# Optimization experiments

Hardware: AMD Instinct MI355X
Metric: run time of the kernel (lower is better)

## Reference

```python
import jax, jax.numpy as jnp
import numpy as np

IN_FEATURES = 4096
OUT_FEATURES = 8192
LUT_SIZE = 65536  # 256 * 256 two-level codebook


def setup_inputs() -> dict:
    key = jax.random.key(0)
    k_x, k_b, k_f, k_s, k_l = jax.random.split(key, 5)
    x = jax.random.normal(k_x, (2, 256, IN_FEATURES), dtype=jnp.float32)
    base_idx = jax.random.randint(k_b, (OUT_FEATURES, IN_FEATURES), 0, 256, dtype=jnp.int32)
    fine_idx = jax.random.randint(k_f, (OUT_FEATURES, IN_FEATURES), 0, 256, dtype=jnp.int32)
    scale = jax.random.uniform(k_s, (OUT_FEATURES, 1), dtype=jnp.float32)
    lut = jax.random.normal(k_l, (LUT_SIZE,), dtype=jnp.float32)
    return {"x": x, "base_idx": base_idx, "fine_idx": fine_idx, "scale": scale, "lut": lut}


def reference(x, base_idx, fine_idx, scale, lut):
    # Two-level LUT dequant: combined 16-bit index = base*256 + fine
    combined_idx = base_idx * 256 + fine_idx              # [out, in] int32
    weights = lut[combined_idx] * scale                   # [out, in] fp32, per-row scale
    # F.linear(x, weights) == x @ weights.T
    return jnp.einsum('bsi,oi->bso', x, weights)
```

## Files before the change

### kernel.cpp

```cpp
#include <hip/hip_runtime.h>

typedef unsigned short ushort_t;
typedef unsigned int   uint32;
typedef __attribute__((ext_vector_type(8)))  short short8;
typedef __attribute__((ext_vector_type(4)))  float floatx4;
typedef __attribute__((ext_vector_type(16))) float floatx16;

#define IN_F   4096
#define OUT_F  8192
#define M_TOT  512

__device__ __forceinline__ ushort_t f2bf(float f) {
    uint32 u = __builtin_bit_cast(uint32, f);
    u += 0x7FFFu + ((u >> 16) & 1u);
    return (ushort_t)(u >> 16);
}
__device__ __forceinline__ uint32 pack2bf(float a, float b) {
    return (uint32)f2bf(a) | ((uint32)f2bf(b) << 16);
}

__global__ void cvt_x_kernel(const float* __restrict__ x, ushort_t* __restrict__ xb) {
    const int g  = blockIdx.x * 256 + threadIdx.x;
    const int r  = g >> 9;
    const int k0 = (g & 511) * 8;
    float4 v0 = *(const float4*)(x + (size_t)r * IN_F + k0);
    float4 v1 = *(const float4*)(x + (size_t)r * IN_F + k0 + 4);
    short8 s;
    s[0] = (short)f2bf(v0.x); s[1] = (short)f2bf(v0.y);
    s[2] = (short)f2bf(v0.z); s[3] = (short)f2bf(v0.w);
    s[4] = (short)f2bf(v1.x); s[5] = (short)f2bf(v1.y);
    s[6] = (short)f2bf(v1.z); s[7] = (short)f2bf(v1.w);
    const int mt = r >> 5;
    const int kt = k0 >> 4;
    ushort_t* dst = xb + ((size_t)(mt * 256 + kt) * 32 + (r & 31)) * 16 + (k0 & 15);
    *(short8*)dst = s;
}

__global__ __launch_bounds__(1024, 4)
void fused_kernel(const ushort_t* __restrict__ xb, const int* __restrict__ base_idx,
                  const int* __restrict__ fine_idx, const float* __restrict__ lut,
                  const float* __restrict__ scale, float* __restrict__ out)
{
    __shared__ ushort_t sh_lut[65536];
    __shared__ ushort_t sh_w[2][32 * 128];

    const int tid  = threadIdx.x;
    const int nblk = blockIdx.x;

    for (int i = tid * 4; i < 65536; i += 4096) {
        float4 v = *(const float4*)(lut + i);
        *(uint32*)&sh_lut[i]     = pack2bf(v.x, v.y);
        *(uint32*)&sh_lut[i + 2] = pack2bf(v.z, v.w);
    }

    const int colr = tid >> 5;
    const int kq   = (tid & 31) * 4;
    const int4* bp = (const int4*)(base_idx + (size_t)(nblk * 32 + colr) * IN_F + kq);
    const int4* fp = (const int4*)(fine_idx + (size_t)(nblk * 32 + colr) * IN_F + kq);

    const int woff = colr * 128 + (((kq >> 3) ^ (colr & 7)) << 3) + (kq & 7);

    const int lane = tid & 63;
    const int wave = tid >> 6;
    const int l31  = lane & 31;
    const int lhi  = lane >> 5;
    const int rx8  = l31 & 7;

    int4 ib0 = bp[0];
    int4 if0 = fp[0];
    int4 Ib  = bp[32];
    int4 If  = fp[32];

    __syncthreads();

    {
        uint32 w0 = (uint32)sh_lut[(ib0.x << 8) + if0.x]
                  | ((uint32)sh_lut[(ib0.y << 8) + if0.y] << 16);
        uint32 w1 = (uint32)sh_lut[(ib0.z << 8) + if0.z]
                  | ((uint32)sh_lut[(ib0.w << 8) + if0.w] << 16);
        uint2 wv; wv.x = w0; wv.y = w1;
        *(uint2*)&sh_w[0][woff] = wv;
    }
    int4 Nb = bp[64];
    int4 Nf = fp[64];

    __syncthreads();

    floatx16 acc = {0.f,0.f,0.f,0.f,0.f,0.f,0.f,0.f,0.f,0.f,0.f,0.f,0.f,0.f,0.f,0.f};

    const ushort_t* abase = xb + (size_t)wave * 256 * 512 + l31 * 16 + lhi * 8;

#pragma unroll 2
    for (int t = 0; t < 32; ++t) {
        const int cur = t & 1;

        short8 a0 = *(const short8*)(abase + (size_t)(t * 8 + 0) * 512);
        short8 a1 = *(const short8*)(abase + (size_t)(t * 8 + 1) * 512);
        short8 a2 = *(const short8*)(abase + (size_t)(t * 8 + 2) * 512);
        short8 a3 = *(const short8*)(abase + (size_t)(t * 8 + 3) * 512);
        short8 a4 = *(const short8*)(abase + (size_t)(t * 8 + 4) * 512);
        short8 a5 = *(const short8*)(abase + (size_t)(t * 8 + 5) * 512);
        short8 a6 = *(const short8*)(abase + (size_t)(t * 8 + 6) * 512);
        short8 a7 = *(const short8*)(abase + (size_t)(t * 8 + 7) * 512);

        const ushort_t* wb = sh_w[cur];
        short8 b0 = *(const short8*)&wb[l31 * 128 + ((( 0 + lhi) ^ rx8) << 3)];
        short8 b1 = *(const short8*)&wb[l31 * 128 + ((( 2 + lhi) ^ rx8) << 3)];
        short8 b2 = *(const short8*)&wb[l31 * 128 + ((( 4 + lhi) ^ rx8) << 3)];
        short8 b3 = *(const short8*)&wb[l31 * 128 + ((( 6 + lhi) ^ rx8) << 3)];
        short8 b4 = *(const short8*)&wb[l31 * 128 + ((( 8 + lhi) ^ rx8) << 3)];
        short8 b5 = *(const short8*)&wb[l31 * 128 + (((10 + lhi) ^ rx8) << 3)];
        short8 b6 = *(const short8*)&wb[l31 * 128 + (((12 + lhi) ^ rx8) << 3)];
        short8 b7 = *(const short8*)&wb[l31 * 128 + (((14 + lhi) ^ rx8) << 3)];

        if (t < 31) {
            uint32 w0 = (uint32)sh_lut[(Ib.x << 8) + If.x]
                      | ((uint32)sh_lut[(Ib.y << 8) + If.y] << 16);
            uint32 w1 = (uint32)sh_lut[(Ib.z << 8) + If.z]
                      | ((uint32)sh_lut[(Ib.w << 8) + If.w] << 16);
            uint2 wv; wv.x = w0; wv.y = w1;
            *(uint2*)&sh_w[cur ^ 1][woff] = wv;
            Ib = Nb; If = Nf;
            if (t + 3 < 32) {
                Nb = bp[(t + 3) * 32];
                Nf = fp[(t + 3) * 32];
            }
        }

        acc = __builtin_amdgcn_mfma_f32_32x32x16_bf16(a0, b0, acc, 0, 0, 0);
        acc = __builtin_amdgcn_mfma_f32_32x32x16_bf16(a1, b1, acc, 0, 0, 0);
        acc = __builtin_amdgcn_mfma_f32_32x32x16_bf16(a2, b2, acc, 0, 0, 0);
        acc = __builtin_amdgcn_mfma_f32_32x32x16_bf16(a3, b3, acc, 0, 0, 0);
        acc = __builtin_amdgcn_mfma_f32_32x32x16_bf16(a4, b4, acc, 0, 0, 0);
        acc = __builtin_amdgcn_mfma_f32_32x32x16_bf16(a5, b5, acc, 0, 0, 0);
        acc = __builtin_amdgcn_mfma_f32_32x32x16_bf16(a6, b6, acc, 0, 0, 0);
        acc = __builtin_amdgcn_mfma_f32_32x32x16_bf16(a7, b7, acc, 0, 0, 0);

        asm volatile("s_waitcnt lgkmcnt(0)" ::: "memory");
        __builtin_amdgcn_sched_barrier(0);
        __builtin_amdgcn_s_barrier();
    }

    const float sc = scale[nblk * 32 + l31];
    float* op = out + (size_t)(nblk * 32 + l31);
    const int rbase = wave * 32 + 4 * lhi;
#pragma unroll
    for (int reg = 0; reg < 16; ++reg) {
        const int row = rbase + (reg & 3) + 8 * (reg >> 2);
        op[(size_t)row * OUT_F] = acc[reg] * sc;
    }
}

#define NB  32
#define FBK 128
#define WS  136
#define NITER (IN_F / FBK)
__global__ __launch_bounds__(1024, 4)
void ghost_kernel(const float* __restrict__ xf,
                  const int* __restrict__ base_idx, const int* __restrict__ fine_idx,
                  const float* __restrict__ scale, const float* __restrict__ lut,
                  float* __restrict__ out)
{
    __shared__ ushort_t sh_lut[65536];
    __shared__ ushort_t sh_w[2][NB * WS];
    const int tid = threadIdx.x;
    const int n0  = blockIdx.x * NB;
    for (int i = tid * 4; i < 65536; i += 1024 * 4) {
        float4 v = *(const float4*)(lut + i);
        sh_lut[i + 0] = f2bf(v.x); sh_lut[i + 1] = f2bf(v.y);
        sh_lut[i + 2] = f2bf(v.z); sh_lut[i + 3] = f2bf(v.w);
    }
    const int sn  = tid >> 5;
    const int skq = (tid & 31) * 4;
    const int* bp = base_idx + (size_t)(n0 + sn) * IN_F + skq;
    const int* fp = fine_idx + (size_t)(n0 + sn) * IN_F + skq;
    __syncthreads();
    int4 pb = *(const int4*)(bp);
    int4 pf = *(const int4*)(fp);
    {
        uint32 w0 = (uint32)sh_lut[(pb.x << 8) + pf.x] | ((uint32)sh_lut[(pb.y << 8) + pf.y] << 16);
        uint32 w1 = (uint32)sh_lut[(pb.z << 8) + pf.z] | ((uint32)sh_lut[(pb.w << 8) + pf.w] << 16);
        uint2 wv; wv.x = w0; wv.y = w1;
        *(uint2*)&sh_w[0][sn * WS + skq] = wv;
    }
    pb = *(const int4*)(bp + FBK);
    pf = *(const int4*)(fp + FBK);
    __syncthreads();
    const int lane = tid & 63;
    const int wave = tid >> 6;
    const int l16  = lane & 15;
    const int quad = lane >> 4;
    floatx4 acc[2][2];
    const floatx4 zero = {0.f, 0.f, 0.f, 0.f};
    acc[0][0] = zero; acc[0][1] = zero; acc[1][0] = zero; acc[1][1] = zero;
    const int mrow = wave * 32 + l16;
    const float* xrowf = xf + (size_t)mrow * IN_F + quad * 8;
    for (int t = 0; t < NITER; ++t) {
        const int k0 = t * FBK;
        {
            uint32 w0 = (uint32)sh_lut[(pb.x << 8) + pf.x] | ((uint32)sh_lut[(pb.y << 8) + pf.y] << 16);
            uint32 w1 = (uint32)sh_lut[(pb.z << 8) + pf.z] | ((uint32)sh_lut[(pb.w << 8) + pf.w] << 16);
            uint2 wv; wv.x = w0; wv.y = w1;
            *(uint2*)&sh_w[(t + 1) & 1][sn * WS + skq] = wv;
        }
        {
            const int kk = (t + 2 < NITER ? t + 2 : NITER - 1) * FBK;
            pb = *(const int4*)(bp + kk);
            pf = *(const int4*)(fp + kk);
        }
        const ushort_t* wb = sh_w[t & 1];
#pragma unroll
        for (int ks = 0; ks < 4; ++ks) {
            const int kk = k0 + ks * 32;
            short8 b0 = *(const short8*)&wb[l16        * WS + ks * 32 + quad * 8];
            short8 b1 = *(const short8*)&wb[(16 + l16) * WS + ks * 32 + quad * 8];
            short8 a0, a1;
            const float* p0 = xrowf + kk;
            const float* p1 = xrowf + (size_t)16 * IN_F + kk;
            float4 u0 = *(const float4*)p0, u1 = *(const float4*)(p0 + 4);
            float4 v0 = *(const float4*)p1, v1 = *(const float4*)(p1 + 4);
            a0[0] = (short)f2bf(u0.x); a0[1] = (short)f2bf(u0.y);
            a0[2] = (short)f2bf(u0.z); a0[3] = (short)f2bf(u0.w);
            a0[4] = (short)f2bf(u1.x); a0[5] = (short)f2bf(u1.y);
            a0[6] = (short)f2bf(u1.z); a0[7] = (short)f2bf(u1.w);
            a1[0] = (short)f2bf(v0.x); a1[1] = (short)f2bf(v0.y);
            a1[2] = (short)f2bf(v0.z); a1[3] = (short)f2bf(v0.w);
            a1[4] = (short)f2bf(v1.x); a1[5] = (short)f2bf(v1.y);
            a1[6] = (short)f2bf(v1.z); a1[7] = (short)f2bf(v1.w);
            acc[0][0] = __builtin_amdgcn_mfma_f32_16x16x32_bf16(a0, b0, acc[0][0], 0, 0, 0);
            acc[0][1] = __builtin_amdgcn_mfma_f32_16x16x32_bf16(a0, b1, acc[0][1], 0, 0, 0);
            acc[1][0] = __builtin_amdgcn_mfma_f32_16x16x32_bf16(a1, b0, acc[1][0], 0, 0, 0);
            acc[1][1] = __builtin_amdgcn_mfma_f32_16x16x32_bf16(a1, b1, acc[1][1], 0, 0, 0);
        }
        __syncthreads();
    }
#pragma unroll
    for (int nf = 0; nf < 2; ++nf) {
        const int col = n0 + nf * 16 + l16;
        const float sc = scale[col];
#pragma unroll
        for (int f = 0; f < 2; ++f) {
            const int r0 = wave * 32 + f * 16 + quad * 4;
#pragma unroll
            for (int r = 0; r < 4; ++r) {
                out[(size_t)(r0 + r) * OUT_F + col] = acc[f][nf][r] * sc;
            }
        }
    }
}

extern "C" void kernel_launch(void* const* d_in, const int* in_sizes, int n_in,
                              void* d_out, int out_size, void* d_ws, size_t ws_size,
                              hipStream_t stream) {
    const float* x      = (const float*)d_in[0];
    const int*   bidx   = (const int*)d_in[1];
    const int*   fidx   = (const int*)d_in[2];
    const float* scale  = (const float*)d_in[3];
    const float* lut    = (const float*)d_in[4];
    float*       out    = (float*)d_out;

    const size_t xb_bytes = (size_t)M_TOT * IN_F * sizeof(ushort_t);

    if (ws_size >= xb_bytes) {
        ushort_t* xbuf = (ushort_t*)d_ws;
        cvt_x_kernel<<<1024, 256, 0, stream>>>(x, xbuf);
        fused_kernel<<<256, 1024, 0, stream>>>(xbuf, bidx, fidx, lut, scale, out);
    } else {
        ghost_kernel<<<OUT_F / NB, 1024, 0, stream>>>(x, bidx, fidx, scale, lut, out);
    }
}
```

Measured before the change: 326.0 us.

## Prefetch next-iteration A fragments into ping-pong registers and prioritize MFMA issue

```diff
diff --git a/kernel.cpp b/kernel.cpp
--- a/kernel.cpp
+++ b/kernel.cpp
@@ -36,6 +36,11 @@
     *(short8*)dst = s;
 }
 
+#define LGKM_BARRIER()                                          \
+    asm volatile("s_waitcnt lgkmcnt(0)" ::: "memory");          \
+    __builtin_amdgcn_sched_barrier(0);                          \
+    __builtin_amdgcn_s_barrier();
+
 __global__ __launch_bounds__(1024, 4)
 void fused_kernel(const ushort_t* __restrict__ xb, const int* __restrict__ base_idx,
                   const int* __restrict__ fine_idx, const float* __restrict__ lut,
@@ -66,12 +71,21 @@
     const int lhi  = lane >> 5;
     const int rx8  = l31 & 7;
 
+    const ushort_t* abase = xb + (size_t)wave * 256 * 512 + l31 * 16 + lhi * 8;
+
     int4 ib0 = bp[0];
     int4 if0 = fp[0];
     int4 Ib  = bp[32];
     int4 If  = fp[32];
-
-    __syncthreads();
+    int4 Nb  = bp[64];
+    int4 Nf  = fp[64];
+
+    short8 aA[8], aB[8];
+#pragma unroll
+    for (int i = 0; i < 8; ++i)
+        aA[i] = *(const short8*)(abase + (size_t)i * 512);
+
+    LGKM_BARRIER();
 
     {
         uint32 w0 = (uint32)sh_lut[(ib0.x << 8) + if0.x]
@@ -81,65 +95,47 @@
         uint2 wv; wv.x = w0; wv.y = w1;
         *(uint2*)&sh_w[0][woff] = wv;
     }
-    int4 Nb = bp[64];
-    int4 Nf = fp[64];
-
-    __syncthreads();
+
+    LGKM_BARRIER();
 
     floatx16 acc = {0.f,0.f,0.f,0.f,0.f,0.f,0.f,0.f,0.f,0.f,0.f,0.f,0.f,0.f,0.f,0.f};
 
-    const ushort_t* abase = xb + (size_t)wave * 256 * 512 + l31 * 16 + lhi * 8;
-
-#pragma unroll 2
-    for (int t = 0; t < 32; ++t) {
-        const int cur = t & 1;
-
-        short8 a0 = *(const short8*)(abase + (size_t)(t * 8 + 0) * 512);
-        short8 a1 = *(const short8*)(abase + (size_t)(t * 8 + 1) * 512);
-        short8 a2 = *(const short8*)(abase + (size_t)(t * 8 + 2) * 512);
-        short8 a3 = *(const short8*)(abase + (size_t)(t * 8 + 3) * 512);
-        short8 a4 = *(const short8*)(abase + (size_t)(t * 8 + 4) * 512);
-        short8 a5 = *(const short8*)(abase + (size_t)(t * 8 + 5) * 512);
-        short8 a6 = *(const short8*)(abase + (size_t)(t * 8 + 6) * 512);
-        short8 a7 = *(const short8*)(abase + (size_t)(t * 8 + 7) * 512);
-
-        const ushort_t* wb = sh_w[cur];
-        short8 b0 = *(const short8*)&wb[l31 * 128 + ((( 0 + lhi) ^ rx8) << 3)];
-        short8 b1 = *(const short8*)&wb[l31 * 128 + ((( 2 + lhi) ^ rx8) << 3)];
-        short8 b2 = *(const short8*)&wb[l31 * 128 + ((( 4 + lhi) ^ rx8) << 3)];
-        short8 b3 = *(const short8*)&wb[l31 * 128 + ((( 6 + lhi) ^ rx8) << 3)];
-        short8 b4 = *(const short8*)&wb[l31 * 128 + ((( 8 + lhi) ^ rx8) << 3)];
-        short8 b5 = *(const short8*)&wb[l31 * 128 + (((10 + lhi) ^ rx8) << 3)];
-        short8 b6 = *(const short8*)&wb[l31 * 128 + (((12 + lhi) ^ rx8) << 3)];
-        short8 b7 = *(const short8*)&wb[l31 * 128 + (((14 + lhi) ^ rx8) << 3)];
-
-        if (t < 31) {
-            uint32 w0 = (uint32)sh_lut[(Ib.x << 8) + If.x]
-                      | ((uint32)sh_lut[(Ib.y << 8) + If.y] << 16);
-            uint32 w1 = (uint32)sh_lut[(Ib.z << 8) + If.z]
-                      | ((uint32)sh_lut[(Ib.w << 8) + If.w] << 16);
-            uint2 wv; wv.x = w0; wv.y = w1;
-            *(uint2*)&sh_w[cur ^ 1][woff] = wv;
-            Ib = Nb; If = Nf;
-            if (t + 3 < 32) {
-                Nb = bp[(t + 3) * 32];
-                Nf = fp[(t + 3) * 32];
-            }
-        }
-
-        acc = __builtin_amdgcn_mfma_f32_32x32x16_bf16(a0, b0, acc, 0, 0, 0);
-        acc = __builtin_amdgcn_mfma_f32_32x32x16_bf16(a1, b1, acc, 0, 0, 0);
-        acc = __builtin_amdgcn_mfma_f32_32x32x16_bf16(a2, b2, acc, 0, 0, 0);
-        acc = __builtin_amdgcn_mfma_f32_32x32x16_bf16(a3, b3, acc, 0, 0, 0);
-        acc = __builtin_amdgcn_mfma_f32_32x32x16_bf16(a4, b4, acc, 0, 0, 0);
-        acc = __builtin_amdgcn_mfma_f32_32x32x16_bf16(a5, b5, acc, 0, 0, 0);
-        acc = __builtin_amdgcn_mfma_f32_32x32x16_bf16(a6, b6, acc, 0, 0, 0);
-        acc = __builtin_amdgcn_mfma_f32_32x32x16_bf16(a7, b7, acc, 0, 0, 0);
-
-        asm volatile("s_waitcnt lgkmcnt(0)" ::: "memory");
-        __builtin_amdgcn_sched_barrier(0);
-        __builtin_amdgcn_s_barrier();
-    }
+#define GBODY(T, AX, AY)                                                       \
+    {                                                                          \
+        const int cur = (T) & 1;                                               \
+        const int tl  = ((T) + 3 < 32) ? (T) + 3 : 31;                         \
+        int4 Tb = bp[tl * 32];                                                 \
+        int4 Tf = fp[tl * 32];                                                 \
+        if ((T) + 1 < 32) {                                                    \
+            _Pragma("unroll")                                                  \
+            for (int i = 0; i < 8; ++i)                                        \
+                AY[i] = *(const short8*)(abase + (size_t)(((T) + 1) * 8 + i) * 512); \
+        }                                                                      \
+        const ushort_t* wb = sh_w[cur];                                        \
+        __builtin_amdgcn_s_setprio(1);                                         \
+        _Pragma("unroll")                                                      \
+        for (int i = 0; i < 8; ++i) {                                          \
+            short8 bfr = *(const short8*)&wb[l31 * 128 + (((2 * i + lhi) ^ rx8) << 3)]; \
+            acc = __builtin_amdgcn_mfma_f32_32x32x16_bf16(AX[i], bfr, acc, 0, 0, 0);    \
+        }                                                                      \
+        __builtin_amdgcn_s_setprio(0);                                         \
+        if ((T) < 31) {                                                        \
+            uint32 w0 = (uint32)sh_lut[(Ib.x << 8) + If.x]                     \
+                      | ((uint32)sh_lut[(Ib.y << 8) + If.y] << 16);            \
+            uint32 w1 = (uint32)sh_lut[(Ib.z << 8) + If.z]                     \
+                      | ((uint32)sh_lut[(Ib.w << 8) + If.w] << 16);            \
+            uint2 wv; wv.x = w0; wv.y = w1;                                    \
+            *(uint2*)&sh_w[cur ^ 1][woff] = wv;                                \
+            Ib = Nb; If = Nf; Nb = Tb; Nf = Tf;                                \
+        }                                                                      \
+        LGKM_BARRIER();                                                        \
+    }
+
+    for (int t = 0; t < 32; t += 2) {
+        GBODY(t, aA, aB)
+        GBODY(t + 1, aB, aA)
+    }
+#undef GBODY
 
     const float sc = scale[nblk * 32 + l31];
     float* op = out + (size_t)(nblk * 32 + l31);
```

After: 331.0 us. Within noise of the previous version (+1.5%).

## Dequantize whole weight strip to global scratch before MFMA loop, drop per-step barriers

Applied to the files above, without the earlier changes.

```diff
diff --git a/kernel.cpp b/kernel.cpp
--- a/kernel.cpp
+++ b/kernel.cpp
@@ -5,6 +5,8 @@
 typedef __attribute__((ext_vector_type(8)))  short short8;
 typedef __attribute__((ext_vector_type(4)))  float floatx4;
 typedef __attribute__((ext_vector_type(16))) float floatx16;
+typedef __attribute__((ext_vector_type(4)))  int   intx4;
+typedef __attribute__((ext_vector_type(4)))  float fltx4;
 
 #define IN_F   4096
 #define OUT_F  8192
@@ -39,61 +41,63 @@
 __global__ __launch_bounds__(1024, 4)
 void fused_kernel(const ushort_t* __restrict__ xb, const int* __restrict__ base_idx,
                   const int* __restrict__ fine_idx, const float* __restrict__ lut,
-                  const float* __restrict__ scale, float* __restrict__ out)
+                  const float* __restrict__ scale, float* __restrict__ out,
+                  ushort_t* __restrict__ wstrip)
 {
     __shared__ ushort_t sh_lut[65536];
-    __shared__ ushort_t sh_w[2][32 * 128];
 
     const int tid  = threadIdx.x;
     const int nblk = blockIdx.x;
 
     for (int i = tid * 4; i < 65536; i += 4096) {
-        float4 v = *(const float4*)(lut + i);
+        fltx4 v = __builtin_nontemporal_load((const fltx4*)(lut + i));
         *(uint32*)&sh_lut[i]     = pack2bf(v.x, v.y);
         *(uint32*)&sh_lut[i + 2] = pack2bf(v.z, v.w);
     }
 
+    ushort_t* strip = wstrip + (size_t)nblk * (32 * IN_F);
+
     const int colr = tid >> 5;
-    const int kq   = (tid & 31) * 4;
-    const int4* bp = (const int4*)(base_idx + (size_t)(nblk * 32 + colr) * IN_F + kq);
-    const int4* fp = (const int4*)(fine_idx + (size_t)(nblk * 32 + colr) * IN_F + kq);
-
-    const int woff = colr * 128 + (((kq >> 3) ^ (colr & 7)) << 3) + (kq & 7);
+    const int lnn  = tid & 31;
+    const int*  bidx_row = base_idx + (size_t)(nblk * 32 + colr) * IN_F;
+    const int*  fidx_row = fine_idx + (size_t)(nblk * 32 + colr) * IN_F;
+
+    __syncthreads();
+
+#pragma unroll 4
+    for (int s = 0; s < 16; ++s) {
+        const int k0 = lnn * 8 + s * 256;
+        intx4 b0 = __builtin_nontemporal_load((const intx4*)(bidx_row + k0));
+        intx4 b1 = __builtin_nontemporal_load((const intx4*)(bidx_row + k0 + 4));
+        intx4 f0 = __builtin_nontemporal_load((const intx4*)(fidx_row + k0));
+        intx4 f1 = __builtin_nontemporal_load((const intx4*)(fidx_row + k0 + 4));
+        uint32 w0 = (uint32)sh_lut[(b0.x << 8) + f0.x]
+                  | ((uint32)sh_lut[(b0.y << 8) + f0.y] << 16);
+        uint32 w1 = (uint32)sh_lut[(b0.z << 8) + f0.z]
+                  | ((uint32)sh_lut[(b0.w << 8) + f0.w] << 16);
+        uint32 w2 = (uint32)sh_lut[(b1.x << 8) + f1.x]
+                  | ((uint32)sh_lut[(b1.y << 8) + f1.y] << 16);
+        uint32 w3 = (uint32)sh_lut[(b1.z << 8) + f1.z]
+                  | ((uint32)sh_lut[(b1.w << 8) + f1.w] << 16);
+        uint4 wv; wv.x = w0; wv.y = w1; wv.z = w2; wv.w = w3;
+        const int kt = k0 >> 4;
+        *(uint4*)(strip + (size_t)(kt * 32 + colr) * 16 + ((k0 >> 3) & 1) * 8) = wv;
+    }
+
+    __syncthreads();
 
     const int lane = tid & 63;
     const int wave = tid >> 6;
     const int l31  = lane & 31;
     const int lhi  = lane >> 5;
-    const int rx8  = l31 & 7;
-
-    int4 ib0 = bp[0];
-    int4 if0 = fp[0];
-    int4 Ib  = bp[32];
-    int4 If  = fp[32];
-
-    __syncthreads();
-
-    {
-        uint32 w0 = (uint32)sh_lut[(ib0.x << 8) + if0.x]
-                  | ((uint32)sh_lut[(ib0.y << 8) + if0.y] << 16);
-        uint32 w1 = (uint32)sh_lut[(ib0.z << 8) + if0.z]
-                  | ((uint32)sh_lut[(ib0.w << 8) + if0.w] << 16);
-        uint2 wv; wv.x = w0; wv.y = w1;
-        *(uint2*)&sh_w[0][woff] = wv;
-    }
-    int4 Nb = bp[64];
-    int4 Nf = fp[64];
-
-    __syncthreads();
 
     floatx16 acc = {0.f,0.f,0.f,0.f,0.f,0.f,0.f,0.f,0.f,0.f,0.f,0.f,0.f,0.f,0.f,0.f};
 
-    const ushort_t* abase = xb + (size_t)wave * 256 * 512 + l31 * 16 + lhi * 8;
+    const ushort_t* abase = xb    + (size_t)wave * 256 * 512 + l31 * 16 + lhi * 8;
+    const ushort_t* bbase = strip + l31 * 16 + lhi * 8;
 
 #pragma unroll 2
     for (int t = 0; t < 32; ++t) {
-        const int cur = t & 1;
-
         short8 a0 = *(const short8*)(abase + (size_t)(t * 8 + 0) * 512);
         short8 a1 = *(const short8*)(abase + (size_t)(t * 8 + 1) * 512);
         short8 a2 = *(const short8*)(abase + (size_t)(t * 8 + 2) * 512);
@@ -102,31 +106,14 @@
         short8 a5 = *(const short8*)(abase + (size_t)(t * 8 + 5) * 512);
         short8 a6 = *(const short8*)(abase + (size_t)(t * 8 + 6) * 512);
         short8 a7 = *(const short8*)(abase + (size_t)(t * 8 + 7) * 512);
-
-        const ushort_t* wb = sh_w[cur];
-        short8 b0 = *(const short8*)&wb[l31 * 128 + ((( 0 + lhi) ^ rx8) << 3)];
-        short8 b1 = *(const short8*)&wb[l31 * 128 + ((( 2 + lhi) ^ rx8) << 3)];
-        short8 b2 = *(const short8*)&wb[l31 * 128 + ((( 4 + lhi) ^ rx8) << 3)];
-        short8 b3 = *(const short8*)&wb[l31 * 128 + ((( 6 + lhi) ^ rx8) << 3)];
-        short8 b4 = *(const short8*)&wb[l31 * 128 + ((( 8 + lhi) ^ rx8) << 3)];
-        short8 b5 = *(const short8*)&wb[l31 * 128 + (((10 + lhi) ^ rx8) << 3)];
-        short8 b6 = *(const short8*)&wb[l31 * 128 + (((12 + lhi) ^ rx8) << 3)];
-        short8 b7 = *(const short8*)&wb[l31 * 128 + (((14 + lhi) ^ rx8) << 3)];
-
-        if (t < 31) {
-            uint32 w0 = (uint32)sh_lut[(Ib.x << 8) + If.x]
-                      | ((uint32)sh_lut[(Ib.y << 8) + If.y] << 16);
-            uint32 w1 = (uint32)sh_lut[(Ib.z << 8) + If.z]
-                      | ((uint32)sh_lut[(Ib.w << 8) + If.w] << 16);
-            uint2 wv; wv.x = w0; wv.y = w1;
-            *(uint2*)&sh_w[cur ^ 1][woff] = wv;
-            Ib = Nb; If = Nf;
-            if (t + 3 < 32) {
-                Nb = bp[(t + 3) * 32];
-                Nf = fp[(t + 3) * 32];
-            }
-        }
-
+        short8 b0 = *(const short8*)(bbase + (size_t)(t * 8 + 0) * 512);
+        short8 b1 = *(const short8*)(bbase + (size_t)(t * 8 + 1) * 512);
+        short8 b2 = *(const short8*)(bbase + (size_t)(t * 8 + 2) * 512);
+        short8 b3 = *(const short8*)(bbase + (size_t)(t * 8 + 3) * 512);
+        short8 b4 = *(const short8*)(bbase + (size_t)(t * 8 + 4) * 512);
+        short8 b5 = *(const short8*)(bbase + (size_t)(t * 8 + 5) * 512);
+        short8 b6 = *(const short8*)(bbase + (size_t)(t * 8 + 6) * 512);
+        short8 b7 = *(const short8*)(bbase + (size_t)(t * 8 + 7) * 512);
         acc = __builtin_amdgcn_mfma_f32_32x32x16_bf16(a0, b0, acc, 0, 0, 0);
         acc = __builtin_amdgcn_mfma_f32_32x32x16_bf16(a1, b1, acc, 0, 0, 0);
         acc = __builtin_amdgcn_mfma_f32_32x32x16_bf16(a2, b2, acc, 0, 0, 0);
@@ -135,10 +122,6 @@
         acc = __builtin_amdgcn_mfma_f32_32x32x16_bf16(a5, b5, acc, 0, 0, 0);
         acc = __builtin_amdgcn_mfma_f32_32x32x16_bf16(a6, b6, acc, 0, 0, 0);
         acc = __builtin_amdgcn_mfma_f32_32x32x16_bf16(a7, b7, acc, 0, 0, 0);
-
-        asm volatile("s_waitcnt lgkmcnt(0)" ::: "memory");
-        __builtin_amdgcn_sched_barrier(0);
-        __builtin_amdgcn_s_barrier();
     }
 
     const float sc = scale[nblk * 32 + l31];
@@ -260,11 +243,13 @@
     float*       out    = (float*)d_out;
 
     const size_t xb_bytes = (size_t)M_TOT * IN_F * sizeof(ushort_t);
-
-    if (ws_size >= xb_bytes) {
+    const size_t wq_bytes = (size_t)OUT_F * IN_F * sizeof(ushort_t);
+
+    if (ws_size >= xb_bytes + wq_bytes) {
         ushort_t* xbuf = (ushort_t*)d_ws;
+        ushort_t* wbuf = (ushort_t*)((char*)d_ws + xb_bytes);
         cvt_x_kernel<<<1024, 256, 0, stream>>>(x, xbuf);
-        fused_kernel<<<256, 1024, 0, stream>>>(xbuf, bidx, fidx, lut, scale, out);
+        fused_kernel<<<256, 1024, 0, stream>>>(xbuf, bidx, fidx, lut, scale, out, wbuf);
     } else {
         ghost_kernel<<<OUT_F / NB, 1024, 0, stream>>>(x, bidx, fidx, scale, lut, out);
     }
```

Result: slower. 367.0 us (+12.6%).
